# Performance work log

Hardware: AMD Instinct MI355X
Metric: run time of the kernel (lower is better)

Reference implementation:

```python
import jax, jax.numpy as jnp
import numpy as np

S = 14
L_COORD = 5.0
L_NOOBJ = 0.5


def setup_inputs() -> dict:
    key = jax.random.key(0)
    k1, k2, k3, k4 = jax.random.split(key, 4)
    N = 4096
    # positive uniforms so sqrt(w), sqrt(h) and IoU areas are well-defined (as in real YOLO outputs)
    pred_tensor = jax.random.uniform(k1, (N, S, S, 30), dtype=jnp.float32, minval=0.01, maxval=1.0)
    target_boxes = jax.random.uniform(k2, (N, S, S, 4), dtype=jnp.float32, minval=0.01, maxval=1.0)
    target_cls = jax.random.uniform(k3, (N, S, S, 20), dtype=jnp.float32)
    has_object_map = jax.random.bernoulli(k4, 0.15, (N, S, S))
    return {"pred_tensor": pred_tensor, "target_boxes": target_boxes,
            "target_cls": target_cls, "has_object_map": has_object_map}


def _xywh2xyxy(b):
    # b: (..., 4) as [cx, cy, w, h]; cx,cy are in grid units -> divide by S
    x, y, w, h = b[..., 0], b[..., 1], b[..., 2], b[..., 3]
    return jnp.stack([x / S - 0.5 * w, y / S - 0.5 * h,
                      x / S + 0.5 * w, y / S + 0.5 * h], axis=-1)


def _iou_pairwise(b1, b2):
    # elementwise IoU between matched boxes (diag of compute_iou), b: (..., 4) xyxy
    lt = jnp.maximum(b1[..., :2], b2[..., :2])
    rb = jnp.minimum(b1[..., 2:], b2[..., 2:])
    wh = jnp.maximum(rb - lt, 0.0)
    inter = wh[..., 0] * wh[..., 1]
    a1 = (b1[..., 2] - b1[..., 0]) * (b1[..., 3] - b1[..., 1])
    a2 = (b2[..., 2] - b2[..., 0]) * (b2[..., 3] - b2[..., 1])
    return inter / (a1 + a2 - inter)


def reference(pred_tensor, target_boxes, target_cls, has_object_map):
    N = pred_tensor.shape[0]
    obj = has_object_map.astype(pred_tensor.dtype)          # (N,S,S)
    noobj = 1.0 - obj

    box1 = pred_tensor[..., 0:5]
    box2 = pred_tensor[..., 5:10]
    pred_cls = pred_tensor[..., 10:]

    # class loss: masked sum-MSE over object cells
    cls_loss = jnp.sum(obj[..., None] * (pred_cls - target_cls) ** 2)

    # no-object loss: confidences of both predictors in non-object cells vs 0
    no_obj_loss = L_NOOBJ * jnp.sum(noobj * (box1[..., 4] ** 2 + box2[..., 4] ** 2))

    # best-of-B selection by IoU against target (elementwise, matched per cell)
    tgt_xyxy = _xywh2xyxy(target_boxes)
    iou1 = _iou_pairwise(_xywh2xyxy(box1[..., :4]), tgt_xyxy)
    iou2 = _iou_pairwise(_xywh2xyxy(box2[..., :4]), tgt_xyxy)
    take1 = iou1 > iou2
    best_iou = jnp.where(take1, iou1, iou2)                  # (N,S,S)
    best_box = jnp.where(take1[..., None], box1, box2)       # (N,S,S,5)

    xy_err = jnp.sum((best_box[..., :2] - target_boxes[..., :2]) ** 2, axis=-1)
    wh_err = jnp.sum((jnp.sqrt(best_box[..., 2:4]) - jnp.sqrt(target_boxes[..., 2:4])) ** 2, axis=-1)
    reg_loss = L_COORD * jnp.sum(obj * (xy_err + wh_err))

    # containing-object confidence loss; target IoU is detached
    contain_loss = jnp.sum(obj * (best_box[..., 4] - jax.lax.stop_gradient(best_iou)) ** 2)

    total = cls_loss + no_obj_loss + contain_loss + reg_loss
    # [total, reg, containing_obj, no_obj, cls], each averaged over batch
    return jnp.stack([total, reg_loss, contain_loss, no_obj_loss, cls_loss]) / N
```

## Files before the change

### kernel.cpp

```cpp
#include <hip/hip_runtime.h>


#define NBATCH   4096
#define CELLS    (NBATCH * 14 * 14)
#define THREADS  256
#define CPB      128
#define NBLK     (CELLS / CPB)
#define L_COORD  5.0f
#define L_NOOBJ  0.5f

__global__ __launch_bounds__(THREADS, 8) void yolo_main(
    const float* __restrict__ pred,
    const float* __restrict__ tbox,
    const float* __restrict__ tcls,
    const int*   __restrict__ objmap,
    float4*      __restrict__ part)
{
    __shared__ float lds_pred[CPB * 30];
    __shared__ float lds_obj[CPB];
    __shared__ float red[4][4];

    const int tid  = threadIdx.x;
    const int blk  = blockIdx.x;
    const int base = blk * CPB;

    {
        const float4* p4  = (const float4*)pred + (size_t)blk * (CPB * 30 / 4);
        float4*       lp4 = (float4*)lds_pred;
        #pragma unroll
        for (int i = tid; i < CPB * 30 / 4; i += THREADS)
            lp4[i] = p4[i];
    }
    if (tid < CPB) lds_obj[tid] = objmap[base + tid] ? 1.0f : 0.0f;
    __syncthreads();

    float acc_reg = 0.f, acc_cont = 0.f, acc_noobj = 0.f, acc_cls = 0.f;

    {
        const float4* c4 = (const float4*)tcls + (size_t)blk * (CPB * 20 / 4);
        #pragma unroll
        for (int i = tid; i < CPB * 20 / 4; i += THREADS) {
            float4 t  = c4[i];
            int cell  = i / 5;
            int ch0   = (i - cell * 5) * 4;
            float o   = lds_obj[cell];
            const float* pc = &lds_pred[cell * 30 + 10 + ch0];
            float d0 = pc[0] - t.x, d1 = pc[1] - t.y;
            float d2 = pc[2] - t.z, d3 = pc[3] - t.w;
            acc_cls += o * (d0*d0 + d1*d1 + d2*d2 + d3*d3);
        }
    }

    {
        const int cell = tid >> 1;
        const int box  = tid & 1;
        const float* pp = &lds_pred[cell * 30 + box * 5];
        float x = pp[0], y = pp[1], w = pp[2], h = pp[3], conf = pp[4];
        float o  = lds_obj[cell];

        acc_noobj = (1.0f - o) * conf * conf;

        float4 tb = ((const float4*)tbox)[base + cell];
        const float invS = 1.0f / 14.0f;

        float txc = tb.x * invS, tyc = tb.y * invS;
        float tx1 = txc - 0.5f * tb.z, ty1 = tyc - 0.5f * tb.w;
        float tx2 = txc + 0.5f * tb.z, ty2 = tyc + 0.5f * tb.w;
        float ta  = (tx2 - tx1) * (ty2 - ty1);

        float ax1 = x * invS - 0.5f * w, ay1 = y * invS - 0.5f * h;
        float ax2 = x * invS + 0.5f * w, ay2 = y * invS + 0.5f * h;
        float a1  = (ax2 - ax1) * (ay2 - ay1);
        float iw  = fmaxf(fminf(ax2, tx2) - fmaxf(ax1, tx1), 0.f);
        float ih  = fmaxf(fminf(ay2, ty2) - fmaxf(ay1, ty1), 0.f);
        float inter = iw * ih;
        float iou   = inter / (a1 + ta - inter);

        float iou_other = __shfl_xor(iou, 1);
        bool win = (box == 0) ? (iou > iou_other) : !(iou_other > iou);

        if (win) {
            float dx = x - tb.x, dy = y - tb.y;
            float dw = sqrtf(w) - sqrtf(tb.z);
            float dh = sqrtf(h) - sqrtf(tb.w);
            acc_reg  = o * (dx*dx + dy*dy + dw*dw + dh*dh);
            float dc = conf - iou;
            acc_cont = o * dc * dc;
        }
    }

    #pragma unroll
    for (int off = 32; off > 0; off >>= 1) {
        acc_reg   += __shfl_down(acc_reg,   off);
        acc_cont  += __shfl_down(acc_cont,  off);
        acc_noobj += __shfl_down(acc_noobj, off);
        acc_cls   += __shfl_down(acc_cls,   off);
    }
    const int wave = tid >> 6, lane = tid & 63;
    if (lane == 0) {
        red[wave][0] = acc_reg;
        red[wave][1] = acc_cont;
        red[wave][2] = acc_noobj;
        red[wave][3] = acc_cls;
    }
    __syncthreads();
    if (tid == 0) {
        float4 p;
        p.x = red[0][0] + red[1][0] + red[2][0] + red[3][0];
        p.y = red[0][1] + red[1][1] + red[2][1] + red[3][1];
        p.z = red[0][2] + red[1][2] + red[2][2] + red[3][2];
        p.w = red[0][3] + red[1][3] + red[2][3] + red[3][3];
        part[blk] = p;
    }
}

__global__ __launch_bounds__(1024) void yolo_reduce(
    const float4* __restrict__ part, float* __restrict__ out)
{
    __shared__ float red[16][4];
    float r = 0.f, c = 0.f, n = 0.f, cl = 0.f;
    for (int i = threadIdx.x; i < NBLK; i += 1024) {
        float4 p = part[i];
        r += p.x; c += p.y; n += p.z; cl += p.w;
    }
    #pragma unroll
    for (int off = 32; off > 0; off >>= 1) {
        r  += __shfl_down(r,  off);
        c  += __shfl_down(c,  off);
        n  += __shfl_down(n,  off);
        cl += __shfl_down(cl, off);
    }
    const int wave = threadIdx.x >> 6, lane = threadIdx.x & 63;
    if (lane == 0) {
        red[wave][0] = r; red[wave][1] = c; red[wave][2] = n; red[wave][3] = cl;
    }
    __syncthreads();
    if (threadIdx.x == 0) {
        float R = 0.f, C = 0.f, Nn = 0.f, Cl = 0.f;
        #pragma unroll
        for (int w = 0; w < 16; ++w) {
            R += red[w][0]; C += red[w][1]; Nn += red[w][2]; Cl += red[w][3];
        }
        const float invN = 1.0f / (float)NBATCH;
        float reg   = L_COORD * R  * invN;
        float cont  =           C  * invN;
        float noobj = L_NOOBJ * Nn * invN;
        float cls   =           Cl * invN;
        out[0] = reg + cont + noobj + cls;
        out[1] = reg;
        out[2] = cont;
        out[3] = noobj;
        out[4] = cls;
    }
}

extern "C" void kernel_launch(void* const* d_in, const int* in_sizes, int n_in,
                              void* d_out, int out_size, void* d_ws, size_t ws_size,
                              hipStream_t stream) {
    const float* pred   = (const float*)d_in[0];
    const float* tbox   = (const float*)d_in[1];
    const float* tcls   = (const float*)d_in[2];
    const int*   objmap = (const int*)  d_in[3];
    float4* part = (float4*)d_ws;
    float*  out  = (float*)d_out;

    yolo_main<<<NBLK, THREADS, 0, stream>>>(pred, tbox, tcls, objmap, part);
    yolo_reduce<<<1, 1024, 0, stream>>>(part, out);
}
```

Baseline: 207.7 us.

## Use persistent per-wave chunks and skip class-target loads for non-object cells

After: 195.7 us. 1.06x faster.

```diff
diff --git a/kernel.cpp b/kernel.cpp
--- a/kernel.cpp
+++ b/kernel.cpp
@@ -4,8 +4,9 @@
 #define NBATCH   4096
 #define CELLS    (NBATCH * 14 * 14)
 #define THREADS  256
-#define CPB      128
-#define NBLK     (CELLS / CPB)
+#define NBLK     2048
+#define NWAVES   (NBLK * 4)
+#define CHUNKS   (CELLS / 32)
 #define L_COORD  5.0f
 #define L_NOOBJ  0.5f
 
@@ -16,76 +17,106 @@
     const int*   __restrict__ objmap,
     float4*      __restrict__ part)
 {
-    __shared__ float lds_pred[CPB * 30];
-    __shared__ float lds_obj[CPB];
+    __shared__ float lds[4 * 960];
     __shared__ float red[4][4];
 
     const int tid  = threadIdx.x;
-    const int blk  = blockIdx.x;
-    const int base = blk * CPB;
-
-    {
-        const float4* p4  = (const float4*)pred + (size_t)blk * (CPB * 30 / 4);
-        float4*       lp4 = (float4*)lds_pred;
-        #pragma unroll
-        for (int i = tid; i < CPB * 30 / 4; i += THREADS)
-            lp4[i] = p4[i];
-    }
-    if (tid < CPB) lds_obj[tid] = objmap[base + tid] ? 1.0f : 0.0f;
-    __syncthreads();
+    const int wv   = tid >> 6;
+    const int lane = tid & 63;
+    float* seg = &lds[wv * 960];
+
+    const int i1  = lane + 64, i2 = lane + 128;
+    const int cc0 = lane / 5;
+    const int cc1 = i1 / 5;
+    const int cc2 = (lane < 32) ? (i2 / 5) : 0;
+    const int ch0a = (lane - cc0 * 5) * 4;
+    const int ch0b = (i1   - cc1 * 5) * 4;
+    const int ch0c = (i2   - cc2 * 5) * 4;
+    const int bcell = lane >> 1;
+    const int box   = lane & 1;
+    const float invS = 1.0f / 14.0f;
 
     float acc_reg = 0.f, acc_cont = 0.f, acc_noobj = 0.f, acc_cls = 0.f;
 
-    {
-        const float4* c4 = (const float4*)tcls + (size_t)blk * (CPB * 20 / 4);
-        #pragma unroll
-        for (int i = tid; i < CPB * 20 / 4; i += THREADS) {
-            float4 t  = c4[i];
-            int cell  = i / 5;
-            int ch0   = (i - cell * 5) * 4;
-            float o   = lds_obj[cell];
-            const float* pc = &lds_pred[cell * 30 + 10 + ch0];
-            float d0 = pc[0] - t.x, d1 = pc[1] - t.y;
-            float d2 = pc[2] - t.z, d3 = pc[3] - t.w;
-            acc_cls += o * (d0*d0 + d1*d1 + d2*d2 + d3*d3);
+    const int gw0 = blockIdx.x * 4 + wv;
+    for (int chunk = gw0; chunk < CHUNKS; chunk += NWAVES) {
+        const size_t cbase = (size_t)chunk * 32;
+
+        const int* ob = objmap + cbase;
+        const int o0  = ob[cc0];
+        const int o1  = ob[cc1];
+        const int o2  = ob[cc2];
+        const int obx = ob[bcell];
+        const float4 tb = ((const float4*)tbox)[cbase + bcell];
+
+        const float4* p4 = (const float4*)pred + (size_t)chunk * 240;
+        float4* s4 = (float4*)seg;
+        float4 v0 = p4[lane];
+        float4 v1 = p4[i1];
+        float4 v2 = p4[i2];
+        float4 v3;
+        if (lane < 48) v3 = p4[lane + 192];
+        s4[lane] = v0;
+        s4[i1]   = v1;
+        s4[i2]   = v2;
+        if (lane < 48) s4[lane + 192] = v3;
+
+        __builtin_amdgcn_s_waitcnt(0);
+
+        {
+            const float4* t4 = (const float4*)tcls + (size_t)chunk * 160;
+            float cl = 0.f;
+            if (o0) {
+                float4 t = t4[lane];
+                const float* pc = &seg[cc0 * 30 + 10 + ch0a];
+                float d0 = pc[0]-t.x, d1 = pc[1]-t.y, d2 = pc[2]-t.z, d3 = pc[3]-t.w;
+                cl += d0*d0 + d1*d1 + d2*d2 + d3*d3;
+            }
+            if (o1) {
+                float4 t = t4[i1];
+                const float* pc = &seg[cc1 * 30 + 10 + ch0b];
+                float d0 = pc[0]-t.x, d1 = pc[1]-t.y, d2 = pc[2]-t.z, d3 = pc[3]-t.w;
+                cl += d0*d0 + d1*d1 + d2*d2 + d3*d3;
+            }
+            if ((lane < 32) && o2) {
+                float4 t = t4[i2];
+                const float* pc = &seg[cc2 * 30 + 10 + ch0c];
+                float d0 = pc[0]-t.x, d1 = pc[1]-t.y, d2 = pc[2]-t.z, d3 = pc[3]-t.w;
+                cl += d0*d0 + d1*d1 + d2*d2 + d3*d3;
+            }
+            acc_cls += cl;
         }
-    }
-
-    {
-        const int cell = tid >> 1;
-        const int box  = tid & 1;
-        const float* pp = &lds_pred[cell * 30 + box * 5];
-        float x = pp[0], y = pp[1], w = pp[2], h = pp[3], conf = pp[4];
-        float o  = lds_obj[cell];
-
-        acc_noobj = (1.0f - o) * conf * conf;
-
-        float4 tb = ((const float4*)tbox)[base + cell];
-        const float invS = 1.0f / 14.0f;
-
-        float txc = tb.x * invS, tyc = tb.y * invS;
-        float tx1 = txc - 0.5f * tb.z, ty1 = tyc - 0.5f * tb.w;
-        float tx2 = txc + 0.5f * tb.z, ty2 = tyc + 0.5f * tb.w;
-        float ta  = (tx2 - tx1) * (ty2 - ty1);
-
-        float ax1 = x * invS - 0.5f * w, ay1 = y * invS - 0.5f * h;
-        float ax2 = x * invS + 0.5f * w, ay2 = y * invS + 0.5f * h;
-        float a1  = (ax2 - ax1) * (ay2 - ay1);
-        float iw  = fmaxf(fminf(ax2, tx2) - fmaxf(ax1, tx1), 0.f);
-        float ih  = fmaxf(fminf(ay2, ty2) - fmaxf(ay1, ty1), 0.f);
-        float inter = iw * ih;
-        float iou   = inter / (a1 + ta - inter);
-
-        float iou_other = __shfl_xor(iou, 1);
-        bool win = (box == 0) ? (iou > iou_other) : !(iou_other > iou);
-
-        if (win) {
-            float dx = x - tb.x, dy = y - tb.y;
-            float dw = sqrtf(w) - sqrtf(tb.z);
-            float dh = sqrtf(h) - sqrtf(tb.w);
-            acc_reg  = o * (dx*dx + dy*dy + dw*dw + dh*dh);
-            float dc = conf - iou;
-            acc_cont = o * dc * dc;
+
+        {
+            const float* pp = &seg[bcell * 30 + box * 5];
+            float x = pp[0], y = pp[1], w = pp[2], h = pp[3], conf = pp[4];
+
+            if (!obx) acc_noobj += conf * conf;
+
+            float txc = tb.x * invS, tyc = tb.y * invS;
+            float tx1 = txc - 0.5f * tb.z, ty1 = tyc - 0.5f * tb.w;
+            float tx2 = txc + 0.5f * tb.z, ty2 = tyc + 0.5f * tb.w;
+            float ta  = (tx2 - tx1) * (ty2 - ty1);
+
+            float ax1 = x * invS - 0.5f * w, ay1 = y * invS - 0.5f * h;
+            float ax2 = x * invS + 0.5f * w, ay2 = y * invS + 0.5f * h;
+            float a1  = (ax2 - ax1) * (ay2 - ay1);
+            float iw  = fmaxf(fminf(ax2, tx2) - fmaxf(ax1, tx1), 0.f);
+            float ih  = fmaxf(fminf(ay2, ty2) - fmaxf(ay1, ty1), 0.f);
+            float inter = iw * ih;
+            float iou   = inter / (a1 + ta - inter);
+
+            float iou_other = __shfl_xor(iou, 1);
+            bool win = (box == 0) ? (iou > iou_other) : !(iou_other > iou);
+
+            if (win && obx) {
+                float dx = x - tb.x, dy = y - tb.y;
+                float dw = sqrtf(w) - sqrtf(tb.z);
+                float dh = sqrtf(h) - sqrtf(tb.w);
+                acc_reg  += dx*dx + dy*dy + dw*dw + dh*dh;
+                float dc  = conf - iou;
+                acc_cont += dc * dc;
+            }
         }
     }
 
@@ -96,12 +127,11 @@
         acc_noobj += __shfl_down(acc_noobj, off);
         acc_cls   += __shfl_down(acc_cls,   off);
     }
-    const int wave = tid >> 6, lane = tid & 63;
     if (lane == 0) {
-        red[wave][0] = acc_reg;
-        red[wave][1] = acc_cont;
-        red[wave][2] = acc_noobj;
-        red[wave][3] = acc_cls;
+        red[wv][0] = acc_reg;
+        red[wv][1] = acc_cont;
+        red[wv][2] = acc_noobj;
+        red[wv][3] = acc_cls;
     }
     __syncthreads();
     if (tid == 0) {
@@ -110,7 +140,7 @@
         p.y = red[0][1] + red[1][1] + red[2][1] + red[3][1];
         p.z = red[0][2] + red[1][2] + red[2][2] + red[3][2];
         p.w = red[0][3] + red[1][3] + red[2][3] + red[3][3];
-        part[blk] = p;
+        part[blockIdx.x] = p;
     }
 }
 
@@ -119,6 +149,7 @@
 {
     __shared__ float red[16][4];
     float r = 0.f, c = 0.f, n = 0.f, cl = 0.f;
+    #pragma unroll
     for (int i = threadIdx.x; i < NBLK; i += 1024) {
         float4 p = part[i];
         r += p.x; c += p.y; n += p.z; cl += p.w;
```
